# Optimization experiments

Hardware: AMD Instinct MI355X
Metric: run time of the kernel (lower is better)

The kernel has to match this reference:

```python
import jax, jax.numpy as jnp
import numpy as np

N_RULES = 64  # R
OUT_PER_RULE = 64  # O, fc out = R*O = 4096


def setup_inputs() -> dict:
    key = jax.random.key(0)
    k1, k2, k3, k4 = jax.random.split(key, 4)
    S, D_IN = 8192, 1024
    RO = N_RULES * OUT_PER_RULE
    X = jax.random.normal(k1, (S, D_IN), dtype=jnp.float32)
    # torch.nn.Linear-style weight [out, in] and bias [out]
    W = jax.random.normal(k2, (RO, D_IN), dtype=jnp.float32) * (1.0 / np.sqrt(D_IN))
    b = jax.random.normal(k3, (RO,), dtype=jnp.float32) * 0.01
    # rule firing strengths (computed under no_grad in the original)
    lambdas = jax.random.uniform(k4, (S, N_RULES), dtype=jnp.float32)
    return {"X": X, "W": W, "b": b, "lambdas": lambdas}


def reference(X, W, b, lambdas):
    # fc + sigmoid: [S, R*O]
    H = jax.nn.sigmoid(X @ W.T + b)
    S = H.shape[0]
    # apply_rule_strength: block-diagonal lambda_eye @ H^T is exactly a
    # rule-weighted sum over the R consecutive O-sized blocks of H.
    Hr = H.reshape(S, N_RULES, OUT_PER_RULE)  # [S, R, O]
    Y = jnp.einsum("sr,sro->so", lambdas, Hr)  # [S, O]
    return Y
```

## Files before the change

kernel.cpp:

```cpp
#include <hip/hip_runtime.h>

#define S_DIM 8192
#define K_DIM 1024
#define RO_DIM 4096
#define O_DIM 64
#define SO (S_DIM * O_DIM)

typedef __attribute__((ext_vector_type(8))) __bf16 bf16x8;
typedef __attribute__((ext_vector_type(4))) float floatx4;
typedef __attribute__((ext_vector_type(4))) unsigned short ushx4;

__device__ inline unsigned short f2bf(float f) {
  unsigned u = __builtin_bit_cast(unsigned, f);
  u += 0x7fff + ((u >> 16) & 1);
  return (unsigned short)(u >> 16);
}
__device__ inline float bf2f(unsigned short h) {
  unsigned u = ((unsigned)h) << 16;
  return __builtin_bit_cast(float, u);
}

__global__ __launch_bounds__(256) void cast_kernel(const float* __restrict__ X,
                                                   const float* __restrict__ W,
                                                   unsigned short* __restrict__ Xb,
                                                   unsigned short* __restrict__ Wb) {
  const int NX4 = (S_DIM * K_DIM) / 4;
#pragma unroll
  for (int i = 0; i < 4; ++i) {
    int g = blockIdx.x * 1024 + i * 256 + threadIdx.x;
    float4 v;
    unsigned short* dst;
    if (g < NX4) {
      v = ((const float4*)X)[g];
      dst = Xb + (size_t)g * 4;
    } else {
      int j = g - NX4;
      v = ((const float4*)W)[j];
      dst = Wb + (size_t)j * 4;
    }
    ushx4 o;
    o.x = f2bf(v.x); o.y = f2bf(v.y); o.z = f2bf(v.z); o.w = f2bf(v.w);
    *(ushx4*)dst = o;
  }
}

__global__ __launch_bounds__(256) void gemm_kernel(const unsigned short* __restrict__ Xb,
                                                   const unsigned short* __restrict__ Wb,
                                                   const float* __restrict__ bias,
                                                   const float* __restrict__ lam,
                                                   unsigned short* __restrict__ partial) {
  __shared__ __align__(16) unsigned char smem[33792];
  unsigned short* Atile = (unsigned short*)smem;
  unsigned short* Btile = (unsigned short*)(smem + 16384);
  float* lamsh = (float*)(smem + 32768);

  const int t = threadIdx.x;
  const int lane = t & 63;
  const int w = t >> 6;
  const int wm = w & 1;
  const int oh = w >> 1;
  const int quad = lane >> 4;
  const int l16 = lane & 15;
  const int gm0 = blockIdx.y * 128;
  const int gn0 = blockIdx.x * 128;

  {
    int row = t >> 1, rl = t & 1;
    lamsh[t] = lam[(size_t)(gm0 + row) * 64 + blockIdx.x * 2 + rl];
  }

  floatx4 acc[4][2][2];
#pragma unroll
  for (int rh = 0; rh < 2; ++rh)
#pragma unroll
    for (int ni = 0; ni < 2; ++ni) {
      float bv = bias[gn0 + rh * 64 + oh * 32 + ni * 16 + l16];
#pragma unroll
      for (int mi = 0; mi < 4; ++mi)
        acc[mi][rh][ni] = (floatx4){bv, bv, bv, bv};
    }

  for (int k0 = 0; k0 < K_DIM; k0 += 64) {
    __syncthreads();
#pragma unroll
    for (int i = 0; i < 4; ++i) {
      int idx = i * 256 + t;
      int row = idx >> 3;
      int cc = idx & 7;
      int gcc = cc ^ (row & 7);
      const unsigned short* ga = Xb + (size_t)(gm0 + row) * K_DIM + k0 + gcc * 8;
      const unsigned short* gb = Wb + (size_t)(gn0 + row) * K_DIM + k0 + gcc * 8;
      __builtin_amdgcn_global_load_lds(
          (const __attribute__((address_space(1))) void*)ga,
          (__attribute__((address_space(3))) void*)(Atile + idx * 8), 16, 0, 0);
      __builtin_amdgcn_global_load_lds(
          (const __attribute__((address_space(1))) void*)gb,
          (__attribute__((address_space(3))) void*)(Btile + idx * 8), 16, 0, 0);
    }
    __syncthreads();

#pragma unroll
    for (int s = 0; s < 2; ++s) {
      bf16x8 af[4], bfr[2][2];
#pragma unroll
      for (int mi = 0; mi < 4; ++mi) {
        int row = wm * 64 + mi * 16 + l16;
        int cc = (s * 4 + quad) ^ (row & 7);
        af[mi] = *(const bf16x8*)(Atile + row * 64 + cc * 8);
      }
#pragma unroll
      for (int rh = 0; rh < 2; ++rh)
#pragma unroll
        for (int ni = 0; ni < 2; ++ni) {
          int row = rh * 64 + oh * 32 + ni * 16 + l16;
          int cc = (s * 4 + quad) ^ (row & 7);
          bfr[rh][ni] = *(const bf16x8*)(Btile + row * 64 + cc * 8);
        }
#pragma unroll
      for (int mi = 0; mi < 4; ++mi)
#pragma unroll
        for (int rh = 0; rh < 2; ++rh)
#pragma unroll
          for (int ni = 0; ni < 2; ++ni)
            acc[mi][rh][ni] =
                __builtin_amdgcn_mfma_f32_16x16x32_bf16(af[mi], bfr[rh][ni], acc[mi][rh][ni], 0, 0, 0);
    }
  }

  unsigned short* pbase = partial + (size_t)blockIdx.x * SO + (size_t)gm0 * O_DIM;
#pragma unroll
  for (int mi = 0; mi < 4; ++mi) {
#pragma unroll
    for (int reg = 0; reg < 4; ++reg) {
      int row = wm * 64 + mi * 16 + quad * 4 + reg;
      float2 lv = *(const float2*)(lamsh + row * 2);
#pragma unroll
      for (int ni = 0; ni < 2; ++ni) {
        float h0 = 1.f / (1.f + __expf(-acc[mi][0][ni][reg]));
        float h1 = 1.f / (1.f + __expf(-acc[mi][1][ni][reg]));
        float y = lv.x * h0 + lv.y * h1;
        pbase[(size_t)row * O_DIM + oh * 32 + ni * 16 + l16] = f2bf(y);
      }
    }
  }
}

__global__ __launch_bounds__(256) void reduce_kernel(const unsigned short* __restrict__ partial,
                                                     float* __restrict__ Y) {
  int i4 = blockIdx.x * 256 + threadIdx.x;
  float s0 = 0.f, s1 = 0.f, s2 = 0.f, s3 = 0.f;
#pragma unroll
  for (int c = 0; c < 32; ++c) {
    ushx4 v = ((const ushx4*)(partial + (size_t)c * SO))[i4];
    s0 += bf2f(v.x); s1 += bf2f(v.y); s2 += bf2f(v.z); s3 += bf2f(v.w);
  }
  ((float4*)Y)[i4] = (float4){s0, s1, s2, s3};
}

extern "C" void kernel_launch(void* const* d_in, const int* in_sizes, int n_in,
                              void* d_out, int out_size, void* d_ws, size_t ws_size,
                              hipStream_t stream) {
  const float* X = (const float*)d_in[0];
  const float* W = (const float*)d_in[1];
  const float* b = (const float*)d_in[2];
  const float* lam = (const float*)d_in[3];
  float* Y = (float*)d_out;

  unsigned short* Xb = (unsigned short*)d_ws;
  unsigned short* Wb = Xb + (size_t)S_DIM * K_DIM;
  unsigned short* partial = Wb + (size_t)RO_DIM * K_DIM;

  int nCast = ((S_DIM + RO_DIM) * K_DIM / 4) / 1024;
  cast_kernel<<<nCast, 256, 0, stream>>>(X, W, Xb, Wb);

  dim3 g(RO_DIM / 128, S_DIM / 128);
  gemm_kernel<<<g, 256, 0, stream>>>(Xb, Wb, b, lam, partial);

  reduce_kernel<<<SO / 1024, 256, 0, stream>>>(partial, Y);
}
```

Before: 188.6 us.

## Enlarge GEMM tiles to 256x256 with 8 waves, pipelined staging, in-block rule reduction

The GEMM moves from 128x128 tiles with 4 waves to 256x256 tiles with 8 waves. It uses double-buffered LDS with interleaved global-to-LDS prefetch, per-phase barriers, s_setprio around the MFMA bursts, and a swizzled block order for L2 locality. Each block now covers 4 rules, so the lambda-weighted sigmoid outputs are reduced across the 4 rules inside LDS before writing, which halves the number of partial slices. That cuts the partial traffic and the reduce work, and raises MFMA reuse per loaded byte. In exchange it uses about 132KB of LDS with larger register pressure, and the grid is only 512 blocks.

```diff
diff --git a/kernel.cpp b/kernel.cpp
--- a/kernel.cpp
+++ b/kernel.cpp
@@ -5,10 +5,12 @@
 #define RO_DIM 4096
 #define O_DIM 64
 #define SO (S_DIM * O_DIM)
+#define NSLICE 16
 
 typedef __attribute__((ext_vector_type(8))) __bf16 bf16x8;
 typedef __attribute__((ext_vector_type(4))) float floatx4;
 typedef __attribute__((ext_vector_type(4))) unsigned short ushx4;
+typedef __attribute__((ext_vector_type(8))) unsigned short ushx8;
 
 __device__ inline unsigned short f2bf(float f) {
   unsigned u = __builtin_bit_cast(unsigned, f);
@@ -44,103 +46,192 @@
   }
 }
 
-__global__ __launch_bounds__(256) void gemm_kernel(const unsigned short* __restrict__ Xb,
-                                                   const unsigned short* __restrict__ Wb,
-                                                   const float* __restrict__ bias,
-                                                   const float* __restrict__ lam,
-                                                   unsigned short* __restrict__ partial) {
-  __shared__ __align__(16) unsigned char smem[33792];
-  unsigned short* Atile = (unsigned short*)smem;
-  unsigned short* Btile = (unsigned short*)(smem + 16384);
-  float* lamsh = (float*)(smem + 32768);
+
+template <int MB>
+__device__ __forceinline__ void rdA(bf16x8 (&af)[2][2], const unsigned short* As,
+                                    int cA0, int cA1) {
+  af[0][0] = *(const bf16x8*)(As + MB * 1024 + cA0);
+  af[0][1] = *(const bf16x8*)(As + MB * 1024 + cA1);
+  af[1][0] = *(const bf16x8*)(As + (MB + 1) * 1024 + cA0);
+  af[1][1] = *(const bf16x8*)(As + (MB + 1) * 1024 + cA1);
+}
+
+template <int MB>
+__device__ __forceinline__ void mfma8(floatx4 (&acc)[8][4], const bf16x8 (&af)[2][2],
+                                      const bf16x8 (&bfr)[4][2]) {
+  __builtin_amdgcn_s_setprio(1);
+#pragma unroll
+  for (int ii = 0; ii < 2; ++ii)
+#pragma unroll
+    for (int ni = 0; ni < 4; ++ni) {
+      acc[MB + ii][ni] = __builtin_amdgcn_mfma_f32_16x16x32_bf16(
+          af[ii][0], bfr[ni][0], acc[MB + ii][ni], 0, 0, 0);
+      acc[MB + ii][ni] = __builtin_amdgcn_mfma_f32_16x16x32_bf16(
+          af[ii][1], bfr[ni][1], acc[MB + ii][ni], 0, 0, 0);
+    }
+  __builtin_amdgcn_s_setprio(0);
+}
+
+#define BAR() __builtin_amdgcn_s_barrier()
+#define LGKM0() asm volatile("s_waitcnt lgkmcnt(0)" ::: "memory")
+
+__global__ __launch_bounds__(512, 2) void gemm_kernel(const unsigned short* __restrict__ Xb,
+                                                      const unsigned short* __restrict__ Wb,
+                                                      const float* __restrict__ bias,
+                                                      const float* __restrict__ lam,
+                                                      unsigned short* __restrict__ partial) {
+  __shared__ __align__(16) unsigned char smem[135168];
+  unsigned short* sm = (unsigned short*)smem;
+  float* lamsh = (float*)(smem + 131072);
 
   const int t = threadIdx.x;
   const int lane = t & 63;
   const int w = t >> 6;
-  const int wm = w & 1;
-  const int oh = w >> 1;
+  const int wm = w >> 2;
+  const int wn = w & 3;
   const int quad = lane >> 4;
   const int l16 = lane & 15;
-  const int gm0 = blockIdx.y * 128;
-  const int gn0 = blockIdx.x * 128;
+
+  int id = blockIdx.y * 16 + blockIdx.x;
+  int swz = (id & 7) * 64 + (id >> 3);
+  const int bx = swz & 15;
+  const int by = swz >> 4;
+  const int gm0 = by * 256;
+  const int gn0 = bx * 256;
+
+  const int rowt = t >> 3;
+  const int gcc = (t & 7) ^ (rowt & 7);
+  const size_t goff = (size_t)rowt * K_DIM + (size_t)gcc * 8;
+  const unsigned short* Abase = Xb + (size_t)gm0 * K_DIM;
+  const unsigned short* Bbase = Wb + (size_t)gn0 * K_DIM;
+
+  auto STAGE = [&](const unsigned short* gbase, int half, int ktile, int slotOff) {
+#pragma unroll
+    for (int j = 0; j < 2; ++j) {
+      const unsigned short* src =
+          gbase + (size_t)(half * 128 + j * 64) * K_DIM + ktile * 64 + goff;
+      __builtin_amdgcn_global_load_lds(
+          (const __attribute__((address_space(1))) void*)src,
+          (__attribute__((address_space(3))) void*)(sm + slotOff + j * 4096 + t * 8),
+          16, 0, 0);
+    }
+  };
+
+  STAGE(Abase, 0, 0, 0);
+  STAGE(Abase, 1, 0, 8192);
+  STAGE(Bbase, 0, 0, 16384);
+  STAGE(Bbase, 1, 0, 24576);
+  STAGE(Bbase, 0, 1, 32768 + 16384);
+  STAGE(Bbase, 1, 1, 32768 + 24576);
 
   {
-    int row = t >> 1, rl = t & 1;
-    lamsh[t] = lam[(size_t)(gm0 + row) * 64 + blockIdx.x * 2 + rl];
-  }
-
-  floatx4 acc[4][2][2];
-#pragma unroll
-  for (int rh = 0; rh < 2; ++rh)
-#pragma unroll
-    for (int ni = 0; ni < 2; ++ni) {
-      float bv = bias[gn0 + rh * 64 + oh * 32 + ni * 16 + l16];
-#pragma unroll
-      for (int mi = 0; mi < 4; ++mi)
-        acc[mi][rh][ni] = (floatx4){bv, bv, bv, bv};
-    }
-
-  for (int k0 = 0; k0 < K_DIM; k0 += 64) {
-    __syncthreads();
-#pragma unroll
-    for (int i = 0; i < 4; ++i) {
-      int idx = i * 256 + t;
-      int row = idx >> 3;
-      int cc = idx & 7;
-      int gcc = cc ^ (row & 7);
-      const unsigned short* ga = Xb + (size_t)(gm0 + row) * K_DIM + k0 + gcc * 8;
-      const unsigned short* gb = Wb + (size_t)(gn0 + row) * K_DIM + k0 + gcc * 8;
-      __builtin_amdgcn_global_load_lds(
-          (const __attribute__((address_space(1))) void*)ga,
-          (__attribute__((address_space(3))) void*)(Atile + idx * 8), 16, 0, 0);
-      __builtin_amdgcn_global_load_lds(
-          (const __attribute__((address_space(1))) void*)gb,
-          (__attribute__((address_space(3))) void*)(Btile + idx * 8), 16, 0, 0);
-    }
-    __syncthreads();
-
-#pragma unroll
-    for (int s = 0; s < 2; ++s) {
-      bf16x8 af[4], bfr[2][2];
-#pragma unroll
-      for (int mi = 0; mi < 4; ++mi) {
-        int row = wm * 64 + mi * 16 + l16;
-        int cc = (s * 4 + quad) ^ (row & 7);
-        af[mi] = *(const bf16x8*)(Atile + row * 64 + cc * 8);
+    int i = t;
+    lamsh[i] = lam[(size_t)(gm0 + (i >> 2)) * 64 + bx * 4 + (i & 3)];
+    i = t + 512;
+    lamsh[i] = lam[(size_t)(gm0 + (i >> 2)) * 64 + bx * 4 + (i & 3)];
+  }
+  asm volatile("s_waitcnt vmcnt(4)" ::: "memory");
+  BAR();
+
+  floatx4 acc[8][4];
+#pragma unroll
+  for (int ni = 0; ni < 4; ++ni) {
+    float bv = bias[gn0 + wn * 64 + ni * 16 + l16];
+#pragma unroll
+    for (int mi = 0; mi < 8; ++mi) acc[mi][ni] = (floatx4){bv, bv, bv, bv};
+  }
+
+  const int cA0 = ((quad) ^ (l16 & 7)) * 8;
+  const int cA1 = ((4 + quad) ^ (l16 & 7)) * 8;
+
+  for (int kt = 0; kt < 16; ++kt) {
+    const int b = kt & 1;
+    const unsigned short* As = sm + b * 32768 + wm * 8192 + l16 * 64;
+    const unsigned short* Bs =
+        sm + b * 32768 + 16384 + (wn >> 1) * 8192 + ((wn & 1) * 64 + l16) * 64;
+    const int bufA = ((kt + 1) & 1) * 32768;
+    const int bufB = b * 32768;
+
+    bf16x8 bfr[4][2], af[2][2];
+
+#pragma unroll
+    for (int ni = 0; ni < 4; ++ni) {
+      bfr[ni][0] = *(const bf16x8*)(Bs + ni * 1024 + cA0);
+      bfr[ni][1] = *(const bf16x8*)(Bs + ni * 1024 + cA1);
+    }
+    rdA<0>(af, As, cA0, cA1);
+    if (kt < 15) STAGE(Abase, 0, kt + 1, bufA + 0);
+    BAR();
+    LGKM0();
+    mfma8<0>(acc, af, bfr);
+    BAR();
+
+    rdA<2>(af, As, cA0, cA1);
+    if (kt < 15) STAGE(Abase, 1, kt + 1, bufA + 8192);
+    BAR();
+    LGKM0();
+    mfma8<2>(acc, af, bfr);
+    BAR();
+
+    rdA<4>(af, As, cA0, cA1);
+    if (kt < 14) STAGE(Bbase, 0, kt + 2, bufB + 16384);
+    BAR();
+    LGKM0();
+    mfma8<4>(acc, af, bfr);
+    BAR();
+
+    rdA<6>(af, As, cA0, cA1);
+    if (kt < 14) {
+      STAGE(Bbase, 1, kt + 2, bufB + 24576);
+      asm volatile("s_waitcnt vmcnt(4)" ::: "memory");
+    } else if (kt == 14) {
+      asm volatile("s_waitcnt vmcnt(0)" ::: "memory");
+    }
+    BAR();
+    LGKM0();
+    mfma8<6>(acc, af, bfr);
+    BAR();
+  }
+
+  __syncthreads();
+  {
+    unsigned short* yreg = sm + wn * 16384;
+#pragma unroll
+    for (int mi = 0; mi < 8; ++mi) {
+#pragma unroll
+      for (int r = 0; r < 4; ++r) {
+        int row = wm * 128 + mi * 16 + quad * 4 + r;
+        float lamv = lamsh[row * 4 + wn];
+#pragma unroll
+        for (int ni = 0; ni < 4; ++ni) {
+          float sg = 1.f / (1.f + __expf(-acc[mi][ni][r]));
+          yreg[row * 64 + ((ni ^ quad) * 16) + l16] = f2bf(lamv * sg);
+        }
       }
-#pragma unroll
-      for (int rh = 0; rh < 2; ++rh)
-#pragma unroll
-        for (int ni = 0; ni < 2; ++ni) {
-          int row = rh * 64 + oh * 32 + ni * 16 + l16;
-          int cc = (s * 4 + quad) ^ (row & 7);
-          bfr[rh][ni] = *(const bf16x8*)(Btile + row * 64 + cc * 8);
-        }
-#pragma unroll
-      for (int mi = 0; mi < 4; ++mi)
-#pragma unroll
-        for (int rh = 0; rh < 2; ++rh)
-#pragma unroll
-          for (int ni = 0; ni < 2; ++ni)
-            acc[mi][rh][ni] =
-                __builtin_amdgcn_mfma_f32_16x16x32_bf16(af[mi], bfr[rh][ni], acc[mi][rh][ni], 0, 0, 0);
-    }
-  }
-
-  unsigned short* pbase = partial + (size_t)blockIdx.x * SO + (size_t)gm0 * O_DIM;
-#pragma unroll
-  for (int mi = 0; mi < 4; ++mi) {
-#pragma unroll
-    for (int reg = 0; reg < 4; ++reg) {
-      int row = wm * 64 + mi * 16 + quad * 4 + reg;
-      float2 lv = *(const float2*)(lamsh + row * 2);
-#pragma unroll
-      for (int ni = 0; ni < 2; ++ni) {
-        float h0 = 1.f / (1.f + __expf(-acc[mi][0][ni][reg]));
-        float h1 = 1.f / (1.f + __expf(-acc[mi][1][ni][reg]));
-        float y = lv.x * h0 + lv.y * h1;
-        pbase[(size_t)row * O_DIM + oh * 32 + ni * 16 + l16] = f2bf(y);
+    }
+  }
+  __syncthreads();
+  {
+    unsigned short* pb = partial + (size_t)bx * SO + (size_t)gm0 * 64;
+#pragma unroll
+    for (int g = 0; g < 4; ++g) {
+      int idx = g * 4096 + t * 8;
+      int row = idx >> 6;
+      int c = idx & 63;
+      int phys = row * 64 + ((((c >> 4) ^ ((row >> 2) & 3))) << 4) + (c & 15);
+      float s[8];
+#pragma unroll
+      for (int j = 0; j < 8; ++j) s[j] = 0.f;
+#pragma unroll
+      for (int q = 0; q < 4; ++q) {
+        ushx8 v = *(const ushx8*)(sm + q * 16384 + phys);
+#pragma unroll
+        for (int j = 0; j < 8; ++j) s[j] += bf2f(v[j]);
       }
+      ushx8 o;
+#pragma unroll
+      for (int j = 0; j < 8; ++j) o[j] = f2bf(s[j]);
+      *(ushx8*)(pb + idx) = o;
     }
   }
 }
@@ -150,7 +241,7 @@
   int i4 = blockIdx.x * 256 + threadIdx.x;
   float s0 = 0.f, s1 = 0.f, s2 = 0.f, s3 = 0.f;
 #pragma unroll
-  for (int c = 0; c < 32; ++c) {
+  for (int c = 0; c < NSLICE; ++c) {
     ushx4 v = ((const ushx4*)(partial + (size_t)c * SO))[i4];
     s0 += bf2f(v.x); s1 += bf2f(v.y); s2 += bf2f(v.z); s3 += bf2f(v.w);
   }
@@ -173,8 +264,8 @@
   int nCast = ((S_DIM + RO_DIM) * K_DIM / 4) / 1024;
   cast_kernel<<<nCast, 256, 0, stream>>>(X, W, Xb, Wb);
 
-  dim3 g(RO_DIM / 128, S_DIM / 128);
-  gemm_kernel<<<g, 256, 0, stream>>>(Xb, Wb, b, lam, partial);
+  dim3 g(RO_DIM / 256, S_DIM / 256);
+  gemm_kernel<<<g, 512, 0, stream>>>(Xb, Wb, b, lam, partial);
 
   reduce_kernel<<<SO / 1024, 256, 0, stream>>>(partial, Y);
 }
```

Measured after the change: 167.7 us. -11.1%, faster.
